# Kernel tuning notes

Measured on AMD Instinct MI355X. Metric: run time of the kernel, lower is better.

Reference implementation:

```python
import jax, jax.numpy as jnp
import numpy as np

N_NODES = 100000
IN_F = 128
HID = [128, 128]
EMB = 64
N_EDGES = 3200000


def _glorot(key, fan_in, fan_out):
    lim = np.sqrt(6.0 / (fan_in + fan_out)).astype(np.float32)
    return jax.random.uniform(key, (fan_in, fan_out), jnp.float32, -lim, lim)


def setup_inputs() -> dict:
    key = jax.random.key(0)
    ks = jax.random.split(key, 10)
    h0 = jax.random.normal(ks[0], (N_NODES, IN_F), jnp.float32)
    edge_index = jax.random.randint(ks[1], (2, N_EDGES), 0, N_NODES, jnp.int32)
    edge_weight = jax.random.uniform(ks[2], (N_EDGES,), jnp.float32)
    dims = [(IN_F, HID[0]), (IN_F, HID[0]), (IN_F, HID[0]),
            (HID[0], HID[1]), (HID[0], HID[1]), (HID[1], EMB)]
    out = {"h0": h0, "edge_index": edge_index, "edge_weight": edge_weight}
    for i, (fi, fo) in enumerate(dims):
        out[f"W{i+1}"] = _glorot(ks[3 + i], fi, fo)
        out[f"b{i+1}"] = jnp.zeros((fo,), jnp.float32)
    return out


def gcn_conv(x, W, b, row, col, norm):
    # x: [N,F_in]; row/col/norm already include self-loops and symmetric norm
    h = x @ W                                  # [N, F_out]
    msg = h[row] * norm[:, None]               # gather + scale  [E+N, F_out]
    agg = jax.ops.segment_sum(msg, col, num_segments=x.shape[0])
    return agg + b


def reference(h0, edge_index, edge_weight, W1, b1, W2, b2, W3, b3, W4, b4, W5, b5, W6, b6):
    n = h0.shape[0]
    row, col = edge_index[0], edge_index[1]
    loop = jnp.arange(n, dtype=row.dtype)
    row2 = jnp.concatenate([row, loop])
    col2 = jnp.concatenate([col, loop])
    ew2 = jnp.concatenate([edge_weight, jnp.ones((n,), edge_weight.dtype)])
    # PyG gcn_norm: deg over destination, symmetric D^-1/2 A D^-1/2
    deg = jax.ops.segment_sum(ew2, col2, num_segments=n)
    dis = jnp.where(deg > 0, jax.lax.rsqrt(jnp.maximum(deg, 1e-20)), 0.0)
    norm = dis[row2] * ew2 * dis[col2]

    h1 = jnp.tanh(gcn_conv(h0, W1, b1, row2, col2, norm))
    h2 = jnp.tanh(gcn_conv(h0, W2, b2, row2, col2, norm))
    h3 = jnp.tanh(gcn_conv(h0, W3, b3, row2, col2, norm))
    h123 = h1 * h2 * h3
    h4 = jnp.tanh(gcn_conv(h123, W4, b4, row2, col2, norm))
    h5 = jnp.tanh(gcn_conv(h123, W5, b5, row2, col2, norm))
    h6 = jnp.tanh(gcn_conv(h4 * h5, W6, b6, row2, col2, norm))
    return h6
```

## Files before the change

kernel.cpp:

```cpp
#include <hip/hip_runtime.h>
#include <hip/hip_bf16.h>
#include <hip/hip_fp16.h>

constexpr int FDIM = 128;
#define HSCALE 16384.0f
#define HSCALE_INV (1.0f/16384.0f)
#define ZSCALE 0.125f
#define ZSCALE_COMP (HSCALE_INV * 8.0f)

typedef _Float16 f16x8 __attribute__((ext_vector_type(8)));
typedef float f32x4 __attribute__((ext_vector_type(4)));
typedef unsigned long long ull;

constexpr int CHUNK = 4096;
constexpr int B1 = 64;
constexpr int B2 = 64;
constexpr int NGRP = B1 * B2;
constexpr int MAXC2 = 20;

__global__ __launch_bounds__(256) void k_init(int* __restrict__ cur1,
                                              int* __restrict__ cur2,
                                              int cap1, int cap2)
{
    int i = blockIdx.x * 256 + threadIdx.x;
    if (i < B1) cur1[i] = i * cap1;
    if (i < NGRP) cur2[i] = i * cap2;
}

__global__ __launch_bounds__(256) void k_p1part(const int* __restrict__ col,
                                                const int* __restrict__ row,
                                                const float* __restrict__ ew,
                                                int* __restrict__ cur1,
                                                ull* __restrict__ rec1, int E)
{
    __shared__ ull stage[CHUNK];
    __shared__ int hcnt[B1], lb[B1], gb[B1], lcur[B1];
    int blk = blockIdx.x, t = threadIdx.x;
    if (t < B1) hcnt[t] = 0;
    __syncthreads();
    int base = blk * CHUNK;
    ull rc[16];
    #pragma unroll
    for (int it = 0; it < 16; ++it) {
        int g = base + it * 256 + t;
        if (g < E) {
            int c = col[g], r = row[g];
            rc[it] = ((ull)c << 47) | ((ull)r << 30) |
                     (ull)__half_as_ushort(__float2half(ew[g]));
            atomicAdd(&hcnt[c >> 11], 1);
        } else rc[it] = ~0ull;
    }
    __syncthreads();
    if (t == 0) {
        int run = 0;
        for (int b = 0; b < B1; ++b) { lb[b] = run; run += hcnt[b]; }
    }
    __syncthreads();
    if (t < B1) { lcur[t] = lb[t]; gb[t] = atomicAdd(&cur1[t], hcnt[t]); }
    __syncthreads();
    #pragma unroll
    for (int it = 0; it < 16; ++it) {
        if (rc[it] != ~0ull) {
            int b = (int)(rc[it] >> 58);
            stage[atomicAdd(&lcur[b], 1)] = rc[it];
        }
    }
    __syncthreads();
    int here = min(CHUNK, E - base);
    for (int j = t; j < here; j += 256) {
        ull v = stage[j];
        int b = (int)(v >> 58);
        rec1[gb[b] + (j - lb[b])] = v;
    }
}

__global__ __launch_bounds__(256) void k_p2part(const ull* __restrict__ rec1,
                                                const int* __restrict__ cur1,
                                                int* __restrict__ cur2,
                                                ull* __restrict__ rec2,
                                                int cap1)
{
    __shared__ ull stage[CHUNK];
    __shared__ int hcnt[B2], lb[B2], gb[B2], lcur[B2];
    int b = blockIdx.x / MAXC2, ci = blockIdx.x % MAXC2, t = threadIdx.x;
    int S1 = b * cap1;
    int size = cur1[b] - S1;
    for (int c = ci; c * CHUNK < size; c += MAXC2) {
        int cb = S1 + c * CHUNK;
        int m = min(CHUNK, size - c * CHUNK);
        __syncthreads();
        if (t < B2) hcnt[t] = 0;
        __syncthreads();
        ull rc[16];
        #pragma unroll
        for (int it = 0; it < 16; ++it) {
            int j = it * 256 + t;
            if (j < m) {
                ull v = rec1[cb + j];
                rc[it] = v;
                atomicAdd(&hcnt[(int)((v >> 52) & 63)], 1);
            } else rc[it] = ~0ull;
        }
        __syncthreads();
        if (t == 0) {
            int run = 0;
            for (int s = 0; s < B2; ++s) { lb[s] = run; run += hcnt[s]; }
        }
        __syncthreads();
        if (t < B2) { lcur[t] = lb[t]; gb[t] = atomicAdd(&cur2[b * B2 + t], hcnt[t]); }
        __syncthreads();
        #pragma unroll
        for (int it = 0; it < 16; ++it) {
            if (rc[it] != ~0ull) {
                int s = (int)((rc[it] >> 52) & 63);
                stage[atomicAdd(&lcur[s], 1)] = rc[it];
            }
        }
        __syncthreads();
        for (int j = t; j < m; j += 256) {
            ull v = stage[j];
            int s = (int)((v >> 52) & 63);
            rec2[gb[s] + (j - lb[s])] = v;
        }
    }
}

__global__ __launch_bounds__(1024) void k_gscan(const int* __restrict__ cur2,
                                                int* __restrict__ gbase, int cap2)
{
    __shared__ int s[1024];
    __shared__ int carry;
    int t = threadIdx.x;
    if (t == 0) carry = 0;
    __syncthreads();
    for (int tile = 0; tile < 4; ++tile) {
        int g = tile * 1024 + t;
        int v = cur2[g] - g * cap2;
        s[t] = v;
        __syncthreads();
        for (int o = 1; o < 1024; o <<= 1) {
            int u = (t >= o) ? s[t - o] : 0;
            __syncthreads();
            s[t] += u;
            __syncthreads();
        }
        gbase[g] = carry + s[t] - v;
        __syncthreads();
        if (t == 1023) carry += s[t];
        __syncthreads();
    }
}

__global__ __launch_bounds__(256) void k_p3(const ull* __restrict__ rec2,
                                            const int* __restrict__ cur2,
                                            const int* __restrict__ gbase,
                                            int2* __restrict__ ep, int* __restrict__ off,
                                            float* __restrict__ dis, int cap2, int N, int E)
{
    __shared__ int h[32], lb[32], cur[32];
    __shared__ float dg[32], sdis[32];
    int g = blockIdx.x, t = threadIdx.x;
    int S1 = g * cap2;
    int S2 = cur2[g];
    int base = gbase[g];
    if (t < 32) { h[t] = 0; dg[t] = 0.f; }
    __syncthreads();
    for (int i = S1 + t; i < S2; i += 256) {
        ull rc = rec2[i];
        int nl = (int)((rc >> 47) & 31);
        atomicAdd(&h[nl], 1);
        atomicAdd(&dg[nl], __half2float(__ushort_as_half((unsigned short)(rc & 0xFFFF))));
    }
    __syncthreads();
    if (t == 0) {
        int run = base;
        for (int k = 0; k < 32; ++k) { lb[k] = run; run += h[k]; }
    }
    __syncthreads();
    if (t < 32) {
        cur[t] = lb[t];
        sdis[t] = 1.0f / sqrtf(dg[t] + 1.0f);
        int node = g * 32 + t;
        if (node < N) { off[node] = lb[t]; dis[node] = sdis[t]; }
    }
    if (g == 0 && t == 0) off[N] = E;
    __syncthreads();
    for (int i = S1 + t; i < S2; i += 256) {
        ull rc = rec2[i];
        int nl = (int)((rc >> 47) & 31);
        int p = atomicAdd(&cur[nl], 1);
        float w = __half2float(__ushort_as_half((unsigned short)(rc & 0xFFFF))) * sdis[nl];
        ep[p] = make_int2((int)((rc >> 30) & 0x1FFFF), __float_as_int(w));
    }
}

__global__ __launch_bounds__(256) void k_cvt(const float4* __restrict__ in,
                                             const float* __restrict__ dis,
                                             __half2* __restrict__ out, int n4)
{
    int i = blockIdx.x * 256 + threadIdx.x;
    if (i >= n4) return;
    float4 v = in[i];
    float d = dis[i >> 5];
    __half2 a = __floats2half2_rn(v.x * d, v.y * d);
    __half2 b = __floats2half2_rn(v.z * d, v.w * d);
    float2 pk;
    ((__half2*)&pk)[0] = a;
    ((__half2*)&pk)[1] = b;
    *(float2*)&out[(size_t)i * 2] = pk;
}

__global__ __launch_bounds__(256) void k_wtall(const float* __restrict__ W1, const float* __restrict__ W2,
                                               const float* __restrict__ W3, const float* __restrict__ W4,
                                               const float* __restrict__ W5, const float* __restrict__ W6,
                                               __half* __restrict__ T1, __half* __restrict__ T2,
                                               __half* __restrict__ T3, __half* __restrict__ T4,
                                               __half* __restrict__ T5, __half* __restrict__ T6)
{
    int idx = blockIdx.x * 256 + threadIdx.x;
    const float* W; __half* T; int local, nf;
    if (idx < 81920) {
        int seg = idx >> 14;
        local = idx & 16383;
        nf = 128;
        const float* Ws[5] = {W1, W2, W3, W4, W5};
        __half* Ts[5] = {T1, T2, T3, T4, T5};
        W = Ws[seg]; T = Ts[seg];
    } else if (idx < 90112) {
        local = idx - 81920;
        nf = 64;
        W = W6; T = T6;
    } else return;
    int n = local >> 7, k = local & 127;
    T[local] = __float2half(W[(size_t)k * nf + n]);
}

__global__ __launch_bounds__(256) void k_spmm(const __half2* __restrict__ Xh,
                                              const int2* __restrict__ ep,
                                              const int* __restrict__ off,
                                              const float* __restrict__ dis,
                                              __half2* __restrict__ Yh, int n)
{
    int gt = blockIdx.x * 256 + threadIdx.x;
    int node = gt >> 6;
    int lane = threadIdx.x & 63;
    if (node >= n) return;

    float sn = dis[node];
    float2 x0 = __half22float2(Xh[(size_t)node * 64 + lane]);
    float a0x = sn * x0.x, a0y = sn * x0.y;
    float a1x = 0.f, a1y = 0.f;
    float a2x = 0.f, a2y = 0.f;
    float a3x = 0.f, a3y = 0.f;

    const int e0 = off[node];
    const int cnt = off[node + 1] - e0;
    const int2* el = ep + e0;
    const int nb = cnt >> 2;
    int done = 0;

    if (nb >= 2) {
        int2 q0, q1, q2, q3;
        int2 p0 = el[0], p1 = el[1], p2 = el[2], p3 = el[3];
        q0 = el[4]; q1 = el[5]; q2 = el[6]; q3 = el[7];
        __half2 xc0 = Xh[(size_t)p0.x * 64 + lane];
        __half2 xc1 = Xh[(size_t)p1.x * 64 + lane];
        __half2 xc2 = Xh[(size_t)p2.x * 64 + lane];
        __half2 xc3 = Xh[(size_t)p3.x * 64 + lane];
        float wc0 = __int_as_float(p0.y), wc1 = __int_as_float(p1.y);
        float wc2 = __int_as_float(p2.y), wc3 = __int_as_float(p3.y);

        int b;
        #pragma unroll 2
        for (b = 0; b + 2 < nb; ++b) {
            __half2 xn0 = Xh[(size_t)q0.x * 64 + lane];
            __half2 xn1 = Xh[(size_t)q1.x * 64 + lane];
            __half2 xn2 = Xh[(size_t)q2.x * 64 + lane];
            __half2 xn3 = Xh[(size_t)q3.x * 64 + lane];
            float wn0 = __int_as_float(q0.y), wn1 = __int_as_float(q1.y);
            float wn2 = __int_as_float(q2.y), wn3 = __int_as_float(q3.y);
            const int2* eb = el + (size_t)(b + 2) * 4;
            q0 = eb[0]; q1 = eb[1]; q2 = eb[2]; q3 = eb[3];
            float2 f0 = __half22float2(xc0), f1 = __half22float2(xc1);
            float2 f2 = __half22float2(xc2), f3 = __half22float2(xc3);
            a0x += wc0 * f0.x; a0y += wc0 * f0.y;
            a1x += wc1 * f1.x; a1y += wc1 * f1.y;
            a2x += wc2 * f2.x; a2y += wc2 * f2.y;
            a3x += wc3 * f3.x; a3y += wc3 * f3.y;
            xc0 = xn0; xc1 = xn1; xc2 = xn2; xc3 = xn3;
            wc0 = wn0; wc1 = wn1; wc2 = wn2; wc3 = wn3;
        }
        __half2 xn0 = Xh[(size_t)q0.x * 64 + lane];
        __half2 xn1 = Xh[(size_t)q1.x * 64 + lane];
        __half2 xn2 = Xh[(size_t)q2.x * 64 + lane];
        __half2 xn3 = Xh[(size_t)q3.x * 64 + lane];
        float wn0 = __int_as_float(q0.y), wn1 = __int_as_float(q1.y);
        float wn2 = __int_as_float(q2.y), wn3 = __int_as_float(q3.y);
        {
            float2 f0 = __half22float2(xc0), f1 = __half22float2(xc1);
            float2 f2 = __half22float2(xc2), f3 = __half22float2(xc3);
            a0x += wc0 * f0.x; a0y += wc0 * f0.y;
            a1x += wc1 * f1.x; a1y += wc1 * f1.y;
            a2x += wc2 * f2.x; a2y += wc2 * f2.y;
            a3x += wc3 * f3.x; a3y += wc3 * f3.y;
        }
        {
            float2 f0 = __half22float2(xn0), f1 = __half22float2(xn1);
            float2 f2 = __half22float2(xn2), f3 = __half22float2(xn3);
            a0x += wn0 * f0.x; a0y += wn0 * f0.y;
            a1x += wn1 * f1.x; a1y += wn1 * f1.y;
            a2x += wn2 * f2.x; a2y += wn2 * f2.y;
            a3x += wn3 * f3.x; a3y += wn3 * f3.y;
        }
        done = nb * 4;
    }
    for (int e = done; e < cnt; ++e) {
        int2 p = el[e];
        float2 xv = __half22float2(Xh[(size_t)p.x * 64 + lane]);
        float w = __int_as_float(p.y);
        a0x += w * xv.x; a0y += w * xv.y;
    }
    float rx = (a0x + a1x) + (a2x + a3x);
    float ry = (a0y + a1y) + (a2y + a3y);
    Yh[(size_t)node * 64 + lane] = __floats2half2_rn(rx, ry);
}

__global__ __launch_bounds__(256) void k_spmm64(const __half* __restrict__ Zh,
                                                const int2* __restrict__ ep,
                                                const int* __restrict__ off,
                                                const float* __restrict__ dis,
                                                const float* __restrict__ b6,
                                                float* __restrict__ out, int n)
{
    int gt = blockIdx.x * 256 + threadIdx.x;
    int node = gt >> 6;
    int lane = threadIdx.x & 63;
    if (node >= n) return;
    const int grp = lane >> 4;
    const int l15 = lane & 15;
    const char* Zb = (const char*)Zh;
    const unsigned loff = (unsigned)l15 << 3;

    f32x4 acc0 = {0.f, 0.f, 0.f, 0.f};
    f32x4 acc1 = {0.f, 0.f, 0.f, 0.f};

    if (grp == 0) {
        float sn = dis[node];
        float2 raw = *(const float2*)(Zb + (((unsigned)node << 7) + loff));
        float2 f0 = __half22float2(((const __half2*)&raw)[0]);
        float2 f1 = __half22float2(((const __half2*)&raw)[1]);
        acc0[0] = sn * f0.x; acc0[1] = sn * f0.y;
        acc0[2] = sn * f1.x; acc0[3] = sn * f1.y;
    }

    const int e0 = off[node];
    const int cnt = off[node + 1] - e0;
    const int2* el = ep + e0;
    const int nb = cnt >> 2;
    int done = 0;

    if (nb >= 2) {
        int2 ec = el[grp];
        float2 xc = *(const float2*)(Zb + (((unsigned)ec.x << 7) + loff));
        int2 en = el[4 + grp];
        float2 xn;

        #pragma unroll 2
        for (int b = 0; b + 2 < nb; ++b) {
            xn = *(const float2*)(Zb + (((unsigned)en.x << 7) + loff));
            int2 e2 = el[(b + 2) * 4 + grp];
            float w = __int_as_float(ec.y);
            float2 f0 = __half22float2(((const __half2*)&xc)[0]);
            float2 f1 = __half22float2(((const __half2*)&xc)[1]);
            if (b & 1) {
                acc1[0] += w * f0.x; acc1[1] += w * f0.y;
                acc1[2] += w * f1.x; acc1[3] += w * f1.y;
            } else {
                acc0[0] += w * f0.x; acc0[1] += w * f0.y;
                acc0[2] += w * f1.x; acc0[3] += w * f1.y;
            }
            ec = en; xc = xn; en = e2;
        }
        xn = *(const float2*)(Zb + (((unsigned)en.x << 7) + loff));
        {
            float w = __int_as_float(ec.y);
            float2 f0 = __half22float2(((const __half2*)&xc)[0]);
            float2 f1 = __half22float2(((const __half2*)&xc)[1]);
            acc0[0] += w * f0.x; acc0[1] += w * f0.y;
            acc0[2] += w * f1.x; acc0[3] += w * f1.y;
        }
        {
            float w = __int_as_float(en.y);
            float2 f0 = __half22float2(((const __half2*)&xn)[0]);
            float2 f1 = __half22float2(((const __half2*)&xn)[1]);
            acc1[0] += w * f0.x; acc1[1] += w * f0.y;
            acc1[2] += w * f1.x; acc1[3] += w * f1.y;
        }
        done = nb * 4;
    }
    for (int e = done; e < cnt; e += 4) {
        int idx = e + grp;
        int2 pe = el[min(idx, cnt - 1)];
        float w = (idx < cnt) ? __int_as_float(pe.y) : 0.f;
        float2 raw = *(const float2*)(Zb + (((unsigned)pe.x << 7) + loff));
        float2 f0 = __half22float2(((const __half2*)&raw)[0]);
        float2 f1 = __half22float2(((const __half2*)&raw)[1]);
        acc0[0] += w * f0.x; acc0[1] += w * f0.y;
        acc0[2] += w * f1.x; acc0[3] += w * f1.y;
    }

    f32x4 r;
    #pragma unroll
    for (int j = 0; j < 4; ++j) {
        r[j] = acc0[j] + acc1[j];
        r[j] += __shfl_xor(r[j], 16);
        r[j] += __shfl_xor(r[j], 32);
    }
    if (lane < 16) {
        float4 bb = *(const float4*)(b6 + 4 * l15);
        float4 o;
        o.x = tanhf(fmaf(r[0], ZSCALE_COMP, bb.x));
        o.y = tanhf(fmaf(r[1], ZSCALE_COMP, bb.y));
        o.z = tanhf(fmaf(r[2], ZSCALE_COMP, bb.z));
        o.w = tanhf(fmaf(r[3], ZSCALE_COMP, bb.w));
        *(float4*)((char*)out + (((size_t)node << 8) + ((unsigned)l15 << 4))) = o;
    }
}

__device__ __forceinline__ float fast_tanh(float x) {
    float e = __expf(2.0f * x);
    return 1.0f - 2.0f * __builtin_amdgcn_rcpf(e + 1.0f);
}

template <int FOUT, int NW, bool ACT>
__global__ __launch_bounds__(256, 2) void k_mgemm(const __half* __restrict__ Yh,
                                                  float IS, float OS,
                                                  const float* __restrict__ dis,
                                                  const __half* __restrict__ Wt0, const float* __restrict__ B0,
                                                  const __half* __restrict__ Wt1, const float* __restrict__ B1,
                                                  const __half* __restrict__ Wt2, const float* __restrict__ B2,
                                                  __half* __restrict__ Out, int nRows)
{
    constexpr int NF = FOUT / 16;
    constexpr int FPW = NF / 4;
    int tid = threadIdx.x;
    int wv = tid >> 6;
    int lane = tid & 63;
    int lo = lane & 15, hi = lane >> 4;
    int r0 = blockIdx.x * 64;

    const __half* Wts[3] = {Wt0, Wt1, Wt2};
    const float*  Bs[3]  = {B0, B1, B2};

    f16x8 bfr[FPW][NW][4];
    float bias[FPW][NW];
    #pragma unroll
    for (int fp = 0; fp < FPW; ++fp) {
        int f = wv * FPW + fp;
        #pragma unroll
        for (int w = 0; w < NW; ++w) {
            const __half* Bp = Wts[w] + (size_t)(f * 16 + lo) * 128 + hi * 8;
            #pragma unroll
            for (int ks = 0; ks < 4; ++ks)
                bfr[fp][w][ks] = *(const f16x8*)(Bp + ks * 32);
            if constexpr (ACT) bias[fp][w] = Bs[w][f * 16 + lo];
        }
    }

    float disr[4][4];
    if constexpr (ACT) {
        #pragma unroll
        for (int rt = 0; rt < 4; ++rt)
            #pragma unroll
            for (int r = 0; r < 4; ++r) {
                int row = r0 + rt * 16 + hi * 4 + r;
                if (row >= nRows) row = nRows - 1;
                disr[rt][r] = dis[row];
            }
    }

    f16x8 a[4], an[4];
    {
        int row = r0 + lo;
        if (row >= nRows) row = nRows - 1;
        const __half* Ap = Yh + (size_t)row * 128 + hi * 8;
        #pragma unroll
        for (int ks = 0; ks < 4; ++ks) a[ks] = *(const f16x8*)(Ap + ks * 32);
    }

    #pragma unroll
    for (int rt = 0; rt < 4; ++rt) {
        if (rt < 3) {
            int row = r0 + (rt + 1) * 16 + lo;
            if (row >= nRows) row = nRows - 1;
            const __half* Ap = Yh + (size_t)row * 128 + hi * 8;
            #pragma unroll
            for (int ks = 0; ks < 4; ++ks) an[ks] = *(const f16x8*)(Ap + ks * 32);
        }
        #pragma unroll
        for (int fp = 0; fp < FPW; ++fp) {
            f32x4 ac0 = {0.f, 0.f, 0.f, 0.f};
            f32x4 ac1 = {0.f, 0.f, 0.f, 0.f};
            f32x4 ac2 = {0.f, 0.f, 0.f, 0.f};
            #pragma unroll
            for (int ks = 0; ks < 4; ++ks) {
                ac0 = __builtin_amdgcn_mfma_f32_16x16x32_f16(a[ks], bfr[fp][0][ks], ac0, 0, 0, 0);
                if constexpr (NW > 1)
                    ac1 = __builtin_amdgcn_mfma_f32_16x16x32_f16(a[ks], bfr[fp][1][ks], ac1, 0, 0, 0);
                if constexpr (NW > 2)
                    ac2 = __builtin_amdgcn_mfma_f32_16x16x32_f16(a[ks], bfr[fp][2][ks], ac2, 0, 0, 0);
            }
            int c = (wv * FPW + fp) * 16 + lo;
            #pragma unroll
            for (int r = 0; r < 4; ++r) {
                int row = r0 + rt * 16 + hi * 4 + r;
                float v;
                if constexpr (ACT) {
                    v = fast_tanh(fmaf(ac0[r], IS, bias[fp][0]));
                    if constexpr (NW > 1) v *= fast_tanh(fmaf(ac1[r], IS, bias[fp][1]));
                    if constexpr (NW > 2) v *= fast_tanh(fmaf(ac2[r], IS, bias[fp][2]));
                    v *= OS * disr[rt][r];
                } else {
                    v = ac0[r] * OS;
                }
                if (row < nRows)
                    Out[(size_t)row * FOUT + c] = __float2half(v);
            }
        }
        #pragma unroll
        for (int ks = 0; ks < 4; ++ks) a[ks] = an[ks];
    }
}

extern "C" void kernel_launch(void* const* d_in, const int* in_sizes, int n_in,
                              void* d_out, int out_size, void* d_ws, size_t ws_size,
                              hipStream_t stream)
{
    const float* h0 = (const float*)d_in[0];
    const int*   ei = (const int*)d_in[1];
    const float* ew = (const float*)d_in[2];
    const float* W1 = (const float*)d_in[3];  const float* b1 = (const float*)d_in[4];
    const float* W2 = (const float*)d_in[5];  const float* b2 = (const float*)d_in[6];
    const float* W3 = (const float*)d_in[7];  const float* b3 = (const float*)d_in[8];
    const float* W4 = (const float*)d_in[9];  const float* b4 = (const float*)d_in[10];
    const float* W5 = (const float*)d_in[11]; const float* b5 = (const float*)d_in[12];
    const float* W6 = (const float*)d_in[13]; const float* b6 = (const float*)d_in[14];

    const int N = in_sizes[0] / FDIM;
    const int E = in_sizes[2];
    const int* rowp = ei;
    const int* colp = ei + E;

    const int NB1 = (E + CHUNK - 1) / CHUNK;
    const int cap1 = E / 40;
    const int cap2 = E / 2000;

    char* p = (char*)d_ws;
    auto alloc = [&](size_t bytes) -> void* {
        void* r = (void*)p;
        p += (bytes + 255) & ~(size_t)255;
        return r;
    };
    int* cur1  = (int*)alloc((size_t)B1 * 4);
    int* cur2  = (int*)alloc((size_t)NGRP * 4);
    int* gbase = (int*)alloc((size_t)(NGRP + 1) * 4);
    int* off   = (int*)alloc((size_t)(N + 1) * 4);
    float* dis = (float*)alloc((size_t)N * 4);
    ull* rec1  = (ull*)alloc((size_t)B1 * cap1 * 8);
    ull* rec2  = (ull*)alloc((size_t)NGRP * cap2 * 8);
    __half2* Xh = (__half2*)alloc((size_t)N * FDIM * 2);
    __half2* Hh = (__half2*)alloc((size_t)N * FDIM * 2);
    __half* W1t = (__half*)alloc((size_t)128 * 128 * 2);
    __half* W2t = (__half*)alloc((size_t)128 * 128 * 2);
    __half* W3t = (__half*)alloc((size_t)128 * 128 * 2);
    __half* W4t = (__half*)alloc((size_t)128 * 128 * 2);
    __half* W5t = (__half*)alloc((size_t)128 * 128 * 2);
    __half* W6t = (__half*)alloc((size_t)64 * 128 * 2);

    int2*    ep = (int2*)rec1;
    __half2* Yh = (__half2*)rec2;
    __half*  Zh = (__half*)Xh;

    k_init<<<(NGRP + 255) / 256, 256, 0, stream>>>(cur1, cur2, cap1, cap2);
    k_p1part<<<NB1, 256, 0, stream>>>(colp, rowp, ew, cur1, rec1, E);
    k_p2part<<<B1 * MAXC2, 256, 0, stream>>>(rec1, cur1, cur2, rec2, cap1);
    k_gscan<<<1, 1024, 0, stream>>>(cur2, gbase, cap2);
    k_p3<<<NGRP, 256, 0, stream>>>(rec2, cur2, gbase, ep, off, dis, cap2, N, E);

    k_cvt<<<(N * 32 + 255) / 256, 256, 0, stream>>>((const float4*)h0, dis, Xh, N * 32);
    k_wtall<<<352, 256, 0, stream>>>(W1, W2, W3, W4, W5, W6, W1t, W2t, W3t, W4t, W5t, W6t);

    const int sb = (N + 3) / 4;
    const int gb = (N + 63) / 64;

    k_spmm<<<sb, 256, 0, stream>>>(Xh, ep, off, dis, Yh, N);
    k_mgemm<128, 3, true><<<gb, 256, 0, stream>>>((const __half*)Yh, 1.0f, HSCALE, dis,
        W1t, b1, W2t, b2, W3t, b3, (__half*)Hh, N);
    k_spmm<<<sb, 256, 0, stream>>>(Hh, ep, off, dis, Yh, N);
    k_mgemm<128, 2, true><<<gb, 256, 0, stream>>>((const __half*)Yh, HSCALE_INV, HSCALE, dis,
        W4t, b4, W5t, b5, nullptr, nullptr, (__half*)Hh, N);
    k_mgemm<64, 1, false><<<gb, 256, 0, stream>>>((const __half*)Hh, 1.0f, ZSCALE, nullptr,
        W6t, b6, nullptr, nullptr, nullptr, nullptr, Zh, N);
    k_spmm64<<<sb, 256, 0, stream>>>(Zh, ep, off, dis, b6, (float*)d_out, N);
}
```

Before: 492.8 us.

## Replace group prefix scan with atomic base allocation and fuse prep kernels

Removes the single-block prefix-scan kernel. Each k_p3 block now reserves its output range with an atomicAdd on a global counter, and per-node (start,end) pairs are stored as int2 so the CSR stays consistent even though groups land in non-sorted order. k_p3 also keeps its records in registers (up to 8 per thread) instead of reading rec2 twice. The fp16 input conversion and the weight transpose are merged into one launch. This drops a serialized low-parallelism kernel and two launches, at the cost of non-deterministic edge-segment placement and a hard cap of 2048 records per group.

```diff
diff --git a/kernel.cpp b/kernel.cpp
--- a/kernel.cpp
+++ b/kernel.cpp
@@ -20,11 +20,13 @@
 
 __global__ __launch_bounds__(256) void k_init(int* __restrict__ cur1,
                                               int* __restrict__ cur2,
+                                              int* __restrict__ gtot,
                                               int cap1, int cap2)
 {
     int i = blockIdx.x * 256 + threadIdx.x;
     if (i < B1) cur1[i] = i * cap1;
     if (i < NGRP) cur2[i] = i * cap2;
+    if (i == 0) gtot[0] = 0;
 }
 
 __global__ __launch_bounds__(256) void k_p1part(const int* __restrict__ col,
@@ -125,119 +127,102 @@
     }
 }
 
-__global__ __launch_bounds__(1024) void k_gscan(const int* __restrict__ cur2,
-                                                int* __restrict__ gbase, int cap2)
-{
-    __shared__ int s[1024];
-    __shared__ int carry;
-    int t = threadIdx.x;
-    if (t == 0) carry = 0;
-    __syncthreads();
-    for (int tile = 0; tile < 4; ++tile) {
-        int g = tile * 1024 + t;
-        int v = cur2[g] - g * cap2;
-        s[t] = v;
-        __syncthreads();
-        for (int o = 1; o < 1024; o <<= 1) {
-            int u = (t >= o) ? s[t - o] : 0;
-            __syncthreads();
-            s[t] += u;
-            __syncthreads();
-        }
-        gbase[g] = carry + s[t] - v;
-        __syncthreads();
-        if (t == 1023) carry += s[t];
-        __syncthreads();
-    }
-}
-
 __global__ __launch_bounds__(256) void k_p3(const ull* __restrict__ rec2,
                                             const int* __restrict__ cur2,
-                                            const int* __restrict__ gbase,
-                                            int2* __restrict__ ep, int* __restrict__ off,
-                                            float* __restrict__ dis, int cap2, int N, int E)
+                                            int* __restrict__ gtot,
+                                            int2* __restrict__ ep, int2* __restrict__ off2,
+                                            float* __restrict__ dis, int cap2, int N)
 {
     __shared__ int h[32], lb[32], cur[32];
     __shared__ float dg[32], sdis[32];
+    __shared__ int sbase;
     int g = blockIdx.x, t = threadIdx.x;
     int S1 = g * cap2;
-    int S2 = cur2[g];
-    int base = gbase[g];
+    int size = cur2[g] - S1;
     if (t < 32) { h[t] = 0; dg[t] = 0.f; }
     __syncthreads();
-    for (int i = S1 + t; i < S2; i += 256) {
-        ull rc = rec2[i];
-        int nl = (int)((rc >> 47) & 31);
-        atomicAdd(&h[nl], 1);
-        atomicAdd(&dg[nl], __half2float(__ushort_as_half((unsigned short)(rc & 0xFFFF))));
+    ull rc[8];
+    #pragma unroll
+    for (int it = 0; it < 8; ++it) {
+        int j = it * 256 + t;
+        if (j < size) {
+            ull v = rec2[S1 + j];
+            rc[it] = v;
+            int nl = (int)((v >> 47) & 31);
+            atomicAdd(&h[nl], 1);
+            atomicAdd(&dg[nl], __half2float(__ushort_as_half((unsigned short)(v & 0xFFFF))));
+        } else rc[it] = ~0ull;
     }
     __syncthreads();
     if (t == 0) {
-        int run = base;
+        sbase = atomicAdd(gtot, size);
+        int run = 0;
         for (int k = 0; k < 32; ++k) { lb[k] = run; run += h[k]; }
     }
     __syncthreads();
     if (t < 32) {
-        cur[t] = lb[t];
+        int b0 = sbase + lb[t];
+        cur[t] = b0;
         sdis[t] = 1.0f / sqrtf(dg[t] + 1.0f);
         int node = g * 32 + t;
-        if (node < N) { off[node] = lb[t]; dis[node] = sdis[t]; }
-    }
-    if (g == 0 && t == 0) off[N] = E;
-    __syncthreads();
-    for (int i = S1 + t; i < S2; i += 256) {
-        ull rc = rec2[i];
-        int nl = (int)((rc >> 47) & 31);
-        int p = atomicAdd(&cur[nl], 1);
-        float w = __half2float(__ushort_as_half((unsigned short)(rc & 0xFFFF))) * sdis[nl];
-        ep[p] = make_int2((int)((rc >> 30) & 0x1FFFF), __float_as_int(w));
-    }
-}
-
-__global__ __launch_bounds__(256) void k_cvt(const float4* __restrict__ in,
-                                             const float* __restrict__ dis,
-                                             __half2* __restrict__ out, int n4)
-{
-    int i = blockIdx.x * 256 + threadIdx.x;
-    if (i >= n4) return;
-    float4 v = in[i];
-    float d = dis[i >> 5];
-    __half2 a = __floats2half2_rn(v.x * d, v.y * d);
-    __half2 b = __floats2half2_rn(v.z * d, v.w * d);
-    float2 pk;
-    ((__half2*)&pk)[0] = a;
-    ((__half2*)&pk)[1] = b;
-    *(float2*)&out[(size_t)i * 2] = pk;
-}
-
-__global__ __launch_bounds__(256) void k_wtall(const float* __restrict__ W1, const float* __restrict__ W2,
-                                               const float* __restrict__ W3, const float* __restrict__ W4,
-                                               const float* __restrict__ W5, const float* __restrict__ W6,
-                                               __half* __restrict__ T1, __half* __restrict__ T2,
-                                               __half* __restrict__ T3, __half* __restrict__ T4,
-                                               __half* __restrict__ T5, __half* __restrict__ T6)
-{
-    int idx = blockIdx.x * 256 + threadIdx.x;
-    const float* W; __half* T; int local, nf;
-    if (idx < 81920) {
-        int seg = idx >> 14;
-        local = idx & 16383;
-        nf = 128;
-        const float* Ws[5] = {W1, W2, W3, W4, W5};
-        __half* Ts[5] = {T1, T2, T3, T4, T5};
-        W = Ws[seg]; T = Ts[seg];
-    } else if (idx < 90112) {
-        local = idx - 81920;
-        nf = 64;
-        W = W6; T = T6;
-    } else return;
-    int n = local >> 7, k = local & 127;
-    T[local] = __float2half(W[(size_t)k * nf + n]);
+        if (node < N) { off2[node] = make_int2(b0, b0 + h[t]); dis[node] = sdis[t]; }
+    }
+    __syncthreads();
+    #pragma unroll
+    for (int it = 0; it < 8; ++it) {
+        if (rc[it] != ~0ull) {
+            int nl = (int)((rc[it] >> 47) & 31);
+            int p = atomicAdd(&cur[nl], 1);
+            float w = __half2float(__ushort_as_half((unsigned short)(rc[it] & 0xFFFF))) * sdis[nl];
+            ep[p] = make_int2((int)((rc[it] >> 30) & 0x1FFFF), __float_as_int(w));
+        }
+    }
+}
+
+__global__ __launch_bounds__(256) void k_prep(const float4* __restrict__ in,
+                                              const float* __restrict__ dis, __half2* __restrict__ out, int n4,
+                                              const float* __restrict__ W1, const float* __restrict__ W2,
+                                              const float* __restrict__ W3, const float* __restrict__ W4,
+                                              const float* __restrict__ W5, const float* __restrict__ W6,
+                                              __half* __restrict__ T1, __half* __restrict__ T2,
+                                              __half* __restrict__ T3, __half* __restrict__ T4,
+                                              __half* __restrict__ T5, __half* __restrict__ T6,
+                                              int cvtBlocks)
+{
+    if ((int)blockIdx.x < cvtBlocks) {
+        int i = blockIdx.x * 256 + threadIdx.x;
+        if (i >= n4) return;
+        float4 v = in[i];
+        float d = dis[i >> 5];
+        __half2 a = __floats2half2_rn(v.x * d, v.y * d);
+        __half2 b = __floats2half2_rn(v.z * d, v.w * d);
+        float2 pk;
+        ((__half2*)&pk)[0] = a;
+        ((__half2*)&pk)[1] = b;
+        *(float2*)&out[(size_t)i * 2] = pk;
+    } else {
+        int idx = (blockIdx.x - cvtBlocks) * 256 + threadIdx.x;
+        const float* W; __half* T; int local, nf;
+        if (idx < 81920) {
+            int seg = idx >> 14;
+            local = idx & 16383;
+            nf = 128;
+            const float* Ws[5] = {W1, W2, W3, W4, W5};
+            __half* Ts[5] = {T1, T2, T3, T4, T5};
+            W = Ws[seg]; T = Ts[seg];
+        } else if (idx < 90112) {
+            local = idx - 81920;
+            nf = 64;
+            W = W6; T = T6;
+        } else return;
+        int n = local >> 7, k = local & 127;
+        T[local] = __float2half(W[(size_t)k * nf + n]);
+    }
 }
 
 __global__ __launch_bounds__(256) void k_spmm(const __half2* __restrict__ Xh,
                                               const int2* __restrict__ ep,
-                                              const int* __restrict__ off,
+                                              const int2* __restrict__ off2,
                                               const float* __restrict__ dis,
                                               __half2* __restrict__ Yh, int n)
 {
@@ -253,9 +238,9 @@
     float a2x = 0.f, a2y = 0.f;
     float a3x = 0.f, a3y = 0.f;
 
-    const int e0 = off[node];
-    const int cnt = off[node + 1] - e0;
-    const int2* el = ep + e0;
+    const int2 o2 = off2[node];
+    const int cnt = o2.y - o2.x;
+    const int2* el = ep + o2.x;
     const int nb = cnt >> 2;
     int done = 0;
 
@@ -327,7 +312,7 @@
 
 __global__ __launch_bounds__(256) void k_spmm64(const __half* __restrict__ Zh,
                                                 const int2* __restrict__ ep,
-                                                const int* __restrict__ off,
+                                                const int2* __restrict__ off2,
                                                 const float* __restrict__ dis,
                                                 const float* __restrict__ b6,
                                                 float* __restrict__ out, int n)
@@ -353,9 +338,9 @@
         acc0[2] = sn * f1.x; acc0[3] = sn * f1.y;
     }
 
-    const int e0 = off[node];
-    const int cnt = off[node + 1] - e0;
-    const int2* el = ep + e0;
+    const int2 o2 = off2[node];
+    const int cnt = o2.y - o2.x;
+    const int2* el = ep + o2.x;
     const int nb = cnt >> 2;
     int done = 0;
 
@@ -563,8 +548,8 @@
     };
     int* cur1  = (int*)alloc((size_t)B1 * 4);
     int* cur2  = (int*)alloc((size_t)NGRP * 4);
-    int* gbase = (int*)alloc((size_t)(NGRP + 1) * 4);
-    int* off   = (int*)alloc((size_t)(N + 1) * 4);
+    int* gtot  = (int*)alloc(256);
+    int2* off2 = (int2*)alloc((size_t)N * 8);
     float* dis = (float*)alloc((size_t)N * 4);
     ull* rec1  = (ull*)alloc((size_t)B1 * cap1 * 8);
     ull* rec2  = (ull*)alloc((size_t)NGRP * cap2 * 8);
@@ -581,25 +566,25 @@
     __half2* Yh = (__half2*)rec2;
     __half*  Zh = (__half*)Xh;
 
-    k_init<<<(NGRP + 255) / 256, 256, 0, stream>>>(cur1, cur2, cap1, cap2);
+    k_init<<<(NGRP + 255) / 256, 256, 0, stream>>>(cur1, cur2, gtot, cap1, cap2);
     k_p1part<<<NB1, 256, 0, stream>>>(colp, rowp, ew, cur1, rec1, E);
     k_p2part<<<B1 * MAXC2, 256, 0, stream>>>(rec1, cur1, cur2, rec2, cap1);
-    k_gscan<<<1, 1024, 0, stream>>>(cur2, gbase, cap2);
-    k_p3<<<NGRP, 256, 0, stream>>>(rec2, cur2, gbase, ep, off, dis, cap2, N, E);
-
-    k_cvt<<<(N * 32 + 255) / 256, 256, 0, stream>>>((const float4*)h0, dis, Xh, N * 32);
-    k_wtall<<<352, 256, 0, stream>>>(W1, W2, W3, W4, W5, W6, W1t, W2t, W3t, W4t, W5t, W6t);
+    k_p3<<<NGRP, 256, 0, stream>>>(rec2, cur2, gtot, ep, off2, dis, cap2, N);
+
+    const int cvtBlocks = (N * 32 + 255) / 256;
+    k_prep<<<cvtBlocks + 352, 256, 0, stream>>>((const float4*)h0, dis, Xh, N * 32,
+        W1, W2, W3, W4, W5, W6, W1t, W2t, W3t, W4t, W5t, W6t, cvtBlocks);
 
     const int sb = (N + 3) / 4;
     const int gb = (N + 63) / 64;
 
-    k_spmm<<<sb, 256, 0, stream>>>(Xh, ep, off, dis, Yh, N);
+    k_spmm<<<sb, 256, 0, stream>>>(Xh, ep, off2, dis, Yh, N);
     k_mgemm<128, 3, true><<<gb, 256, 0, stream>>>((const __half*)Yh, 1.0f, HSCALE, dis,
         W1t, b1, W2t, b2, W3t, b3, (__half*)Hh, N);
-    k_spmm<<<sb, 256, 0, stream>>>(Hh, ep, off, dis, Yh, N);
+    k_spmm<<<sb, 256, 0, stream>>>(Hh, ep, off2, dis, Yh, N);
     k_mgemm<128, 2, true><<<gb, 256, 0, stream>>>((const __half*)Yh, HSCALE_INV, HSCALE, dis,
         W4t, b4, W5t, b5, nullptr, nullptr, (__half*)Hh, N);
     k_mgemm<64, 1, false><<<gb, 256, 0, stream>>>((const __half*)Hh, 1.0f, ZSCALE, nullptr,
         W6t, b6, nullptr, nullptr, nullptr, nullptr, Zh, N);
-    k_spmm64<<<sb, 256, 0, stream>>>(Zh, ep, off, dis, b6, (float*)d_out, N);
-}
+    k_spmm64<<<sb, 256, 0, stream>>>(Zh, ep, off2, dis, b6, (float*)d_out, N);
+}
```

Measured after the change: 509.4 us. +3.4%, slower.
